# Kernel tuning notes

Hardware: AMD Instinct MI355X
Metric: run time of the kernel (lower is better)

Reference implementation:

```python
import jax, jax.numpy as jnp
import numpy as np
from functools import partial

D_MODEL, N_HEADS, D_FF, KSIZE = 512, 8, 2048, 31
B, S = 8, 1024
EPS = 1e-5

def layer_norm(x, g, b):
    m = jnp.mean(x, axis=-1, keepdims=True)
    v = jnp.mean(jnp.square(x - m), axis=-1, keepdims=True)
    return (x - m) * jax.lax.rsqrt(v + EPS) * g + b

def ffn(x, ln_g, ln_b, w1, b1, w2, b2):
    h = layer_norm(x, ln_g, ln_b)
    h = jax.nn.silu(h @ w1 + b1) @ w2 + b2
    return x + 0.5 * h

def mhsa(x, ln_g, ln_b, wq, bq, wk, bk, wv, bv, wo, bo):
    b_, s_, d_ = x.shape
    dk = d_ // N_HEADS
    h = layer_norm(x, ln_g, ln_b)
    def heads(y):  # (B,S,D) -> (B,H,S,dk)
        return y.reshape(b_, s_, N_HEADS, dk).transpose(0, 2, 1, 3)
    Q, K, V = heads(h @ wq + bq), heads(h @ wk + bk), heads(h @ wv + bv)
    scores = jnp.einsum('bhqd,bhkd->bhqk', Q, K) / jnp.sqrt(jnp.float32(dk)).astype(x.dtype)
    attn = jax.nn.softmax(scores, axis=-1)
    ctx = jnp.einsum('bhqk,bhkd->bhqd', attn, V)
    ctx = ctx.transpose(0, 2, 1, 3).reshape(b_, s_, d_)
    return x + (ctx @ wo + bo)

def conv_module(x, ln_g, ln_b, pw1_w, pw1_b, dw_w, dw_b, bn_g, bn_b, bn_mean, bn_var, pw2_w, pw2_b):
    h = layer_norm(x, ln_g, ln_b)           # (B,S,D)
    h = h @ pw1_w + pw1_b                   # (B,S,2D) pointwise conv1 (k=1)
    a, g = jnp.split(h, 2, axis=-1)
    h = a * jax.nn.sigmoid(g)               # GLU over channel dim
    hc = h.transpose(0, 2, 1)               # (B,D,S)
    # depthwise conv: kernel (D,1,K), groups=D, SAME padding (K odd)
    hc = jax.lax.conv_general_dilated(
        hc, dw_w, window_strides=(1,), padding='SAME',
        dimension_numbers=('NCH', 'OIH', 'NCH'),
        feature_group_count=D_MODEL) + dw_b[None, :, None]
    # BatchNorm1d (eval mode, running stats)
    hc = (hc - bn_mean[None, :, None]) * jax.lax.rsqrt(bn_var + EPS)[None, :, None]
    hc = hc * bn_g[None, :, None] + bn_b[None, :, None]
    hc = jax.nn.silu(hc)
    hc = jnp.einsum('bcs,co->bos', hc, pw2_w) + pw2_b[None, :, None]  # pointwise conv2
    return x + hc.transpose(0, 2, 1)


def setup_inputs() -> dict:
    key = jax.random.key(0)
    ks = iter(jax.random.split(key, 48))
    def w(shape, scale=0.02):
        return (jax.random.normal(next(ks), shape, dtype=jnp.float32) * scale)
    d, f = D_MODEL, D_FF
    inp = {
        'x': jax.random.normal(next(ks), (B, S, d), dtype=jnp.float32),
        # FFN1
        'ffn1_ln_g': jnp.ones((d,)), 'ffn1_ln_b': jnp.zeros((d,)),
        'ffn1_w1': w((d, f)), 'ffn1_b1': jnp.zeros((f,)),
        'ffn1_w2': w((f, d)), 'ffn1_b2': jnp.zeros((d,)),
        # MHSA
        'mhsa_ln_g': jnp.ones((d,)), 'mhsa_ln_b': jnp.zeros((d,)),
        'wq': w((d, d)), 'bq': jnp.zeros((d,)),
        'wk': w((d, d)), 'bk': jnp.zeros((d,)),
        'wv': w((d, d)), 'bv': jnp.zeros((d,)),
        'wo': w((d, d)), 'bo': jnp.zeros((d,)),
        # Conv module
        'conv_ln_g': jnp.ones((d,)), 'conv_ln_b': jnp.zeros((d,)),
        'pw1_w': w((d, 2 * d)), 'pw1_b': jnp.zeros((2 * d,)),
        'dw_w': w((d, 1, KSIZE)), 'dw_b': jnp.zeros((d,)),
        'bn_g': jnp.ones((d,)), 'bn_b': jnp.zeros((d,)),
        'bn_mean': jnp.zeros((d,)), 'bn_var': jnp.ones((d,)),
        'pw2_w': w((d, d)), 'pw2_b': jnp.zeros((d,)),
        # FFN2
        'ffn2_ln_g': jnp.ones((d,)), 'ffn2_ln_b': jnp.zeros((d,)),
        'ffn2_w1': w((d, f)), 'ffn2_b1': jnp.zeros((f,)),
        'ffn2_w2': w((f, d)), 'ffn2_b2': jnp.zeros((d,)),
        # Final LN
        'final_ln_g': jnp.ones((d,)), 'final_ln_b': jnp.zeros((d,)),
    }
    return inp


def reference(x,
              ffn1_ln_g, ffn1_ln_b, ffn1_w1, ffn1_b1, ffn1_w2, ffn1_b2,
              mhsa_ln_g, mhsa_ln_b, wq, bq, wk, bk, wv, bv, wo, bo,
              conv_ln_g, conv_ln_b, pw1_w, pw1_b, dw_w, dw_b,
              bn_g, bn_b, bn_mean, bn_var, pw2_w, pw2_b,
              ffn2_ln_g, ffn2_ln_b, ffn2_w1, ffn2_b1, ffn2_w2, ffn2_b2,
              final_ln_g, final_ln_b):
    h = ffn(x, ffn1_ln_g, ffn1_ln_b, ffn1_w1, ffn1_b1, ffn1_w2, ffn1_b2)
    h = mhsa(h, mhsa_ln_g, mhsa_ln_b, wq, bq, wk, bk, wv, bv, wo, bo)
    h = conv_module(h, conv_ln_g, conv_ln_b, pw1_w, pw1_b, dw_w, dw_b,
                    bn_g, bn_b, bn_mean, bn_var, pw2_w, pw2_b)
    h = ffn(h, ffn2_ln_g, ffn2_ln_b, ffn2_w1, ffn2_b1, ffn2_w2, ffn2_b2)
    return layer_norm(h, final_ln_g, final_ln_b)
```

## Files before the change

### kernel.cpp

```cpp
#include <hip/hip_runtime.h>
#include <hip/hip_bf16.h>
#include <cstddef>

typedef __hip_bfloat16 bf16;
typedef __attribute__((ext_vector_type(8))) short bf16x8;
typedef __attribute__((ext_vector_type(4))) float f32x4;
typedef __attribute__((ext_vector_type(2))) unsigned int u32x2;

static __device__ __forceinline__ float b2f(bf16 v) { return __bfloat162float(v); }
static __device__ __forceinline__ bf16 f2b(float v) { return __float2bfloat16(v); }
static __device__ __forceinline__ float bits2f(unsigned short u) {
    union { unsigned int i; float f; } c; c.i = ((unsigned int)u) << 16; return c.f;
}
static __device__ __forceinline__ unsigned int f2bu(float v) {
    union { bf16 b; unsigned short u; } c; c.b = f2b(v); return (unsigned int)c.u;
}
static __device__ __forceinline__ float ldx(const void* p, size_t i, bool isbf) {
    return isbf ? b2f(((const bf16*)p)[i]) : ((const float*)p)[i];
}
#define GLOAD_LDS16(g, l)                                                            \
    __builtin_amdgcn_global_load_lds((const __attribute__((address_space(1))) unsigned int*)(g), \
                                     (__attribute__((address_space(3))) unsigned int*)(l), 16, 0, 0)

#define LN_EPS 1e-5f

__global__ void detect_kernel(const void* ones, int* flag) {
    unsigned int w = *(const unsigned int*)ones;
    *flag = (w == 0x3F803F80u) ? 1 : 0;
}

__global__ void to_f32_kernel(const void* x, float* __restrict__ y, int n8, const int* flag) {
    bool isbf = (*flag != 0);
    int i = blockIdx.x * blockDim.x + threadIdx.x;
    if (i >= n8) return;
    size_t base = (size_t)i * 8;
    if (isbf) {
        bf16x8 xv = *(const bf16x8*)((const bf16*)x + base);
#pragma unroll
        for (int u = 0; u < 8; ++u) y[base + u] = bits2f((unsigned short)xv[u]);
    } else {
        f32x4 a = *(const f32x4*)((const float*)x + base);
        f32x4 b = *(const f32x4*)((const float*)x + base + 4);
        *(f32x4*)(y + base) = a;
        *(f32x4*)(y + base + 4) = b;
    }
}

__global__ __launch_bounds__(256) void transpose_kernel(const void* __restrict__ W,
                                                        bf16* __restrict__ Wt,
                                                        int K, int M, const int* flag) {
    bool isbf = (*flag != 0);
    __shared__ float ts[32][33];
    int kt0 = blockIdx.x * 32, mt0 = blockIdx.y * 32;
    int x = threadIdx.x, y = threadIdx.y;
    for (int yy = y; yy < 32; yy += 8)
        ts[yy][x] = ldx(W, (size_t)(kt0 + yy) * M + mt0 + x, isbf);
    __syncthreads();
    for (int yy = y; yy < 32; yy += 8)
        Wt[(size_t)(mt0 + yy) * K + kt0 + x] = f2b(ts[x][yy]);
}

__global__ void bpack_kernel(const void* bq, const void* bk, const void* bv,
                             void* out, const int* flag) {
    bool isbf = (*flag != 0);
    int i = blockIdx.x * blockDim.x + threadIdx.x;
    if (i >= 1536) return;
    const void* src = (i < 512) ? bq : ((i < 1024) ? bk : bv);
    float v = ldx(src, i & 511, isbf);
    if (isbf) ((bf16*)out)[i] = f2b(v);
    else      ((float*)out)[i] = v;
}

__global__ __launch_bounds__(256) void vtrans_kernel(const bf16* __restrict__ P,
                                                     bf16* __restrict__ Vt) {
    __shared__ bf16 t[32][33];
    int s0 = blockIdx.x * 32, c0 = blockIdx.y * 32, b = blockIdx.z;
    int x = threadIdx.x, y = threadIdx.y;
    const bf16* Pb = P + (size_t)b * 1024 * 1536 + 1024;
    bf16* Vtb = Vt + (size_t)b * 512 * 1024;
    for (int yy = y; yy < 32; yy += 8)
        t[yy][x] = Pb[(size_t)(s0 + yy) * 1536 + c0 + x];
    __syncthreads();
    for (int yy = y; yy < 32; yy += 8)
        Vtb[(size_t)(c0 + yy) * 1024 + s0 + x] = t[x][yy];
}

__global__ void glu_kernel(const bf16* __restrict__ u, bf16* __restrict__ o, int n8) {
    int i = blockIdx.x * blockDim.x + threadIdx.x;
    if (i >= n8) return;
    size_t base = (size_t)i * 8;
    int t = (int)(base >> 9), c = (int)(base & 511);
    bf16x8 av = *(const bf16x8*)(u + (size_t)t * 1024 + c);
    bf16x8 gv = *(const bf16x8*)(u + (size_t)t * 1024 + 512 + c);
    __attribute__((aligned(16))) bf16 ov[8];
#pragma unroll
    for (int k = 0; k < 8; ++k) {
        float a = bits2f((unsigned short)av[k]);
        float g = bits2f((unsigned short)gv[k]);
        ov[k] = f2b(a / (1.f + __expf(-g)));
    }
    *(bf16x8*)(o + base) = *(bf16x8*)ov;
}

__global__ __launch_bounds__(256) void ln_kernel(const float* __restrict__ X,
                                                 const void* __restrict__ g,
                                                 const void* __restrict__ b,
                                                 bf16* __restrict__ O, const int* flag) {
    bool isbf = (*flag != 0);
    int tid = threadIdx.x, lane = tid & 63, wid = tid >> 6;
    int t = blockIdx.x * 4 + wid;
    const float* x = X + (size_t)t * 512 + lane * 8;
    __attribute__((aligned(16))) float v[8];
    *(f32x4*)&v[0] = *(const f32x4*)x;
    *(f32x4*)&v[4] = *(const f32x4*)(x + 4);
    float s = 0.f, q = 0.f;
#pragma unroll
    for (int u = 0; u < 8; ++u) { s += v[u]; q += v[u] * v[u]; }
#pragma unroll
    for (int m = 1; m < 64; m <<= 1) { s += __shfl_xor(s, m, 64); q += __shfl_xor(q, m, 64); }
    float mean = s * (1.f / 512.f);
    float var  = q * (1.f / 512.f) - mean * mean;
    float sc = rsqrtf(var + LN_EPS);
    __attribute__((aligned(16))) bf16 ov[8];
#pragma unroll
    for (int u = 0; u < 8; ++u)
        ov[u] = f2b((v[u] - mean) * sc * ldx(g, lane * 8 + u, isbf) + ldx(b, lane * 8 + u, isbf));
    *(bf16x8*)(O + (size_t)t * 512 + lane * 8) = *(bf16x8*)ov;
}

__global__ __launch_bounds__(256) void ln_out_kernel(const float* __restrict__ X,
                                                     const void* __restrict__ g,
                                                     const void* __restrict__ b,
                                                     void* __restrict__ O, const int* flag) {
    bool isbf = (*flag != 0);
    int tid = threadIdx.x, lane = tid & 63, wid = tid >> 6;
    int t = blockIdx.x * 4 + wid;
    const float* x = X + (size_t)t * 512 + lane * 8;
    __attribute__((aligned(16))) float v[8];
    *(f32x4*)&v[0] = *(const f32x4*)x;
    *(f32x4*)&v[4] = *(const f32x4*)(x + 4);
    float s = 0.f, q = 0.f;
#pragma unroll
    for (int u = 0; u < 8; ++u) { s += v[u]; q += v[u] * v[u]; }
#pragma unroll
    for (int m = 1; m < 64; m <<= 1) { s += __shfl_xor(s, m, 64); q += __shfl_xor(q, m, 64); }
    float mean = s * (1.f / 512.f);
    float var  = q * (1.f / 512.f) - mean * mean;
    float sc = rsqrtf(var + LN_EPS);
    float r[8];
#pragma unroll
    for (int u = 0; u < 8; ++u)
        r[u] = (v[u] - mean) * sc * ldx(g, lane * 8 + u, isbf) + ldx(b, lane * 8 + u, isbf);
    size_t off = (size_t)t * 512 + lane * 8;
    if (isbf) {
        __attribute__((aligned(16))) bf16 ov[8];
#pragma unroll
        for (int u = 0; u < 8; ++u) ov[u] = f2b(r[u]);
        *(bf16x8*)((bf16*)O + off) = *(bf16x8*)ov;
    } else {
        *(f32x4*)((float*)O + off) = *(f32x4*)&r[0];
        *(f32x4*)((float*)O + off + 4) = *(f32x4*)&r[4];
    }
}

template <int ACT, int RESADD>
__global__ __launch_bounds__(256) void mgemm_kernel(const bf16* __restrict__ A,
                                                    const bf16* __restrict__ Wt,
                                                    const void* __restrict__ bias,
                                                    bf16* __restrict__ Cb,
                                                    float* __restrict__ res, float alpha,
                                                    int lda, int K, int M, const int* flag) {
    bool isbf = (*flag != 0);
    __shared__ short As[128 * 32];
    __shared__ short Bs[128 * 32];
    int tid = threadIdx.x;
    int rowBase = blockIdx.y * 128, colBase = blockIdx.x * 128;
    int ll = tid & 63, wv = tid >> 6;
    int wr = (wv & 1) * 64, wc = (wv >> 1) * 64;
    int lRow = ll & 15, quad = ll >> 4;

    int sR16 = ll >> 2;
    int kseg = (ll & 3) ^ ((ll >> 3) & 3);
    int segF = quad ^ ((lRow >> 1) & 3);

    f32x4 acc[4][4] = {};

    for (int k0 = 0; k0 < K; k0 += 32) {
#pragma unroll
        for (int j = 0; j < 2; ++j) {
            int rT = wv * 32 + j * 16;
            const bf16* ga = A + (size_t)(rowBase + rT + sR16) * lda + k0 + kseg * 8;
            GLOAD_LDS16(ga, &As[rT * 32]);
            const bf16* gb = Wt + (size_t)(colBase + rT + sR16) * K + k0 + kseg * 8;
            GLOAD_LDS16(gb, &Bs[rT * 32]);
        }
        __syncthreads();
        bf16x8 af[4], bfv[4];
#pragma unroll
        for (int i = 0; i < 4; ++i)
            af[i]  = *(const bf16x8*)&As[(wr + i * 16 + lRow) * 32 + segF * 8];
#pragma unroll
        for (int j = 0; j < 4; ++j)
            bfv[j] = *(const bf16x8*)&Bs[(wc + j * 16 + lRow) * 32 + segF * 8];
#pragma unroll
        for (int i = 0; i < 4; ++i)
#pragma unroll
            for (int j = 0; j < 4; ++j)
                acc[i][j] = __builtin_amdgcn_mfma_f32_16x16x32_bf16(af[i], bfv[j], acc[i][j], 0, 0, 0);
        __syncthreads();
    }

#pragma unroll
    for (int j = 0; j < 4; ++j) {
        int col = colBase + wc + j * 16 + lRow;
        float bv = ldx(bias, col, isbf);
#pragma unroll
        for (int i = 0; i < 4; ++i) {
            int r0 = rowBase + wr + i * 16 + quad * 4;
#pragma unroll
            for (int r = 0; r < 4; ++r) {
                float v = acc[i][j][r] + bv;
                if (ACT == 1) v = v / (1.f + __expf(-v));
                int row = r0 + r;
                if (RESADD) res[(size_t)row * 512 + col] += alpha * v;
                else        Cb[(size_t)row * M + col] = f2b(v);
            }
        }
    }
}

__global__ __launch_bounds__(256) void fattn_kernel(bf16* __restrict__ QO,
                                                    const bf16* __restrict__ Vt) {
    __shared__ short Ks[2][64 * 64];
    __shared__ short Vs[2][64 * 64];
    int tid = threadIdx.x, wid = tid >> 6, ll = tid & 63;
    int n = ll & 15, quad = ll >> 4;
    int id = blockIdx.x;
    int ng = gridDim.x >> 4;
    int g = id % ng, j = id / ng;
    int h = g & 7, b = g >> 3;
    size_t rowB = (size_t)b * 1024;
    int q0 = j * 64 + wid * 16;

    const bf16* Qb = QO + rowB * 1536 + h * 64;
    bf16x8 qf0 = *(const bf16x8*)(Qb + (size_t)(q0 + n) * 1536 + quad * 8);
    bf16x8 qf1 = *(const bf16x8*)(Qb + (size_t)(q0 + n) * 1536 + 32 + quad * 8);

    const bf16* Kb = QO + rowB * 1536 + 512 + h * 64;
    const bf16* Vb = Vt + (size_t)b * 512 * 1024 + (size_t)(h * 64) * 1024;

    int rr = ll >> 3;
    int ch = (ll & 7) ^ rr;

    float l = 0.f;
    f32x4 oacc[4] = {};
    int idxA = (((quad & 1) * 32) + n) * 4;
    int idxB = idxA + 64;
    bool hiC = (quad >= 2);
    int nx = n & 7;
    int sl0 = (quad ^ nx) * 8;
    int sl1 = sl0 ^ (4 * 8);

    auto STAGE = [&](int buf, int k0) {
#pragma unroll
        for (int i2 = 0; i2 < 2; ++i2) {
            int r0 = wid * 16 + i2 * 8;
            const bf16* gk = Kb + (size_t)(k0 + r0 + rr) * 1536 + ch * 8;
            GLOAD_LDS16(gk, &Ks[buf][r0 * 64]);
            const bf16* gv = Vb + (size_t)(r0 + rr) * 1024 + k0 + ch * 8;
            GLOAD_LDS16(gv, &Vs[buf][r0 * 64]);
        }
    };

    auto COMPUTE = [&](const short* Kc, const short* Vc) {
#pragma unroll
        for (int s = 0; s < 2; ++s) {
            const short* kb0 = Kc + (s * 32 + n) * 64;
            const short* kb1 = kb0 + 16 * 64;
            f32x4 s0 = {}, s1 = {};
            s0 = __builtin_amdgcn_mfma_f32_16x16x32_bf16(*(const bf16x8*)(kb0 + sl0), qf0, s0, 0, 0, 0);
            s0 = __builtin_amdgcn_mfma_f32_16x16x32_bf16(*(const bf16x8*)(kb0 + sl1), qf1, s0, 0, 0, 0);
            s1 = __builtin_amdgcn_mfma_f32_16x16x32_bf16(*(const bf16x8*)(kb1 + sl0), qf0, s1, 0, 0, 0);
            s1 = __builtin_amdgcn_mfma_f32_16x16x32_bf16(*(const bf16x8*)(kb1 + sl1), qf1, s1, 0, 0, 0);

            float p0[4], p1[4];
#pragma unroll
            for (int r = 0; r < 4; ++r) {
                p0[r] = __expf(s0[r] * 0.125f);
                p1[r] = __expf(s1[r] * 0.125f);
                l += p0[r] + p1[r];
            }

            int p0d0 = (int)(f2bu(p0[0]) | (f2bu(p0[1]) << 16));
            int p0d1 = (int)(f2bu(p0[2]) | (f2bu(p0[3]) << 16));
            int p1d0 = (int)(f2bu(p1[0]) | (f2bu(p1[1]) << 16));
            int p1d1 = (int)(f2bu(p1[2]) | (f2bu(p1[3]) << 16));
            int a0 = __builtin_amdgcn_ds_bpermute(idxA, p0d0);
            int a1 = __builtin_amdgcn_ds_bpermute(idxA, p0d1);
            int a2 = __builtin_amdgcn_ds_bpermute(idxB, p0d0);
            int a3 = __builtin_amdgcn_ds_bpermute(idxB, p0d1);
            int c0 = __builtin_amdgcn_ds_bpermute(idxA, p1d0);
            int c1 = __builtin_amdgcn_ds_bpermute(idxA, p1d1);
            int c2 = __builtin_amdgcn_ds_bpermute(idxB, p1d0);
            int c3 = __builtin_amdgcn_ds_bpermute(idxB, p1d1);
            union { int d[4]; bf16x8 v; } bf;
            bf.d[0] = hiC ? c0 : a0;
            bf.d[1] = hiC ? c1 : a1;
            bf.d[2] = hiC ? c2 : a2;
            bf.d[3] = hiC ? c3 : a3;

            int vsl = ((s * 4 + quad) ^ nx) * 8;
#pragma unroll
            for (int g2 = 0; g2 < 4; ++g2) {
                const short* vp = Vc + (g2 * 16 + n) * 64 + vsl;
                oacc[g2] = __builtin_amdgcn_mfma_f32_16x16x32_bf16(*(const bf16x8*)vp, bf.v, oacc[g2], 0, 0, 0);
            }
        }
    };

    STAGE(0, 0);
    __syncthreads();
    for (int it = 0; it < 16; it += 2) {
        if (it + 1 < 16) STAGE(1, (it + 1) * 64);
        COMPUTE(&Ks[0][0], &Vs[0][0]);
        __syncthreads();
        if (it + 2 < 16) STAGE(0, (it + 2) * 64);
        COMPUTE(&Ks[1][0], &Vs[1][0]);
        __syncthreads();
    }

    l += __shfl_xor(l, 16, 64);
    l += __shfl_xor(l, 32, 64);
    float linv = 1.f / l;
    bf16* op = QO + (rowB + q0 + n) * 1536 + h * 64 + quad * 4;
#pragma unroll
    for (int g2 = 0; g2 < 4; ++g2) {
        union { bf16 b4[4]; u32x2 w; } ou;
#pragma unroll
        for (int r = 0; r < 4; ++r) ou.b4[r] = f2b(oacc[g2][r] * linv);
        *(u32x2*)(op + g2 * 16) = ou.w;
    }
}

__global__ void dwprep_kernel(const void* __restrict__ w, const void* __restrict__ dwb,
                              const void* __restrict__ bng, const void* __restrict__ bnb,
                              const void* __restrict__ bnm, const void* __restrict__ bnv,
                              bf16* __restrict__ wT, float* __restrict__ scl,
                              float* __restrict__ sft, const int* flag) {
    bool isbf = (*flag != 0);
    int c = blockIdx.x * blockDim.x + threadIdx.x;
    if (c >= 512) return;
    for (int k = 0; k < 31; ++k) wT[k * 512 + c] = f2b(ldx(w, (size_t)c * 31 + k, isbf));
    float s = ldx(bng, c, isbf) * rsqrtf(ldx(bnv, c, isbf) + LN_EPS);
    scl[c] = s;
    sft[c] = (ldx(dwb, c, isbf) - ldx(bnm, c, isbf)) * s + ldx(bnb, c, isbf);
}

__global__ __launch_bounds__(256) void dwconv_kernel(const bf16* __restrict__ X,
                                                     const bf16* __restrict__ wT,
                                                     const float* __restrict__ scl,
                                                     const float* __restrict__ sft,
                                                     bf16* __restrict__ Out) {
    __shared__ bf16 wl[31 * 512];
    __shared__ float sl[512], fl[512];
    int tid = threadIdx.x;
    for (int i = tid; i < (31 * 512) / 8; i += 256)
        *(bf16x8*)&wl[i * 8] = *(const bf16x8*)&wT[i * 8];
    sl[tid] = scl[tid]; sl[tid + 256] = scl[tid + 256];
    fl[tid] = sft[tid]; fl[tid + 256] = sft[tid + 256];
    __syncthreads();

    int lane = tid & 63, sg = tid >> 6;
    int c = lane * 8;
    size_t bOff = (size_t)blockIdx.y * 1024 * 512;
    int sb = blockIdx.x * 16 + sg * 4;

    float acc[4][8] = {};
    for (int kk = 0; kk < 34; ++kk) {
        int sp = sb + kk - 15;
        if (sp < 0 || sp >= 1024) continue;
        bf16x8 xr = *(const bf16x8*)(X + bOff + (size_t)sp * 512 + c);
        float xv[8];
#pragma unroll
        for (int u = 0; u < 8; ++u) xv[u] = bits2f((unsigned short)xr[u]);
#pragma unroll
        for (int o = 0; o < 4; ++o) {
            int kw = kk - o;
            if (kw < 0 || kw > 30) continue;
            bf16x8 wv8 = *(const bf16x8*)&wl[kw * 512 + c];
#pragma unroll
            for (int u = 0; u < 8; ++u) acc[o][u] += xv[u] * bits2f((unsigned short)wv8[u]);
        }
    }
#pragma unroll
    for (int o = 0; o < 4; ++o) {
        __attribute__((aligned(16))) bf16 ov[8];
#pragma unroll
        for (int u = 0; u < 8; ++u) {
            float v = acc[o][u] * sl[c + u] + fl[c + u];
            v = v / (1.f + __expf(-v));
            ov[u] = f2b(v);
        }
        *(bf16x8*)(Out + bOff + (size_t)(sb + o) * 512 + c) = *(bf16x8*)ov;
    }
}

extern "C" void kernel_launch(void* const* d_in, const int* in_sizes, int n_in,
                              void* d_out, int out_size, void* d_ws, size_t ws_size,
                              hipStream_t stream) {
    const int B = 8, S = 1024, D = 512, F = 2048, H = 8;
    const int N = B * S;
    const size_t ND = (size_t)N * D;
    if (n_in < 37) return;

    int idx = 0;
    const void* x          = d_in[idx++];
    const void* ffn1_ln_g  = d_in[idx++];
    const void* ffn1_ln_b  = d_in[idx++];
    const void* ffn1_w1    = d_in[idx++];
    const void* ffn1_b1    = d_in[idx++];
    const void* ffn1_w2    = d_in[idx++];
    const void* ffn1_b2    = d_in[idx++];
    const void* mhsa_ln_g  = d_in[idx++];
    const void* mhsa_ln_b  = d_in[idx++];
    const void* wq         = d_in[idx++];
    const void* bq         = d_in[idx++];
    const void* wk         = d_in[idx++];
    const void* bk         = d_in[idx++];
    const void* wv         = d_in[idx++];
    const void* bv         = d_in[idx++];
    const void* wo         = d_in[idx++];
    const void* bo         = d_in[idx++];
    const void* conv_ln_g  = d_in[idx++];
    const void* conv_ln_b  = d_in[idx++];
    const void* pw1_w      = d_in[idx++];
    const void* pw1_b      = d_in[idx++];
    const void* dw_w       = d_in[idx++];
    const void* dw_b       = d_in[idx++];
    const void* bn_g       = d_in[idx++];
    const void* bn_b       = d_in[idx++];
    const void* bn_mean    = d_in[idx++];
    const void* bn_var     = d_in[idx++];
    const void* pw2_w      = d_in[idx++];
    const void* pw2_b      = d_in[idx++];
    const void* ffn2_ln_g  = d_in[idx++];
    const void* ffn2_ln_b  = d_in[idx++];
    const void* ffn2_w1    = d_in[idx++];
    const void* ffn2_b1    = d_in[idx++];
    const void* ffn2_w2    = d_in[idx++];
    const void* ffn2_b2    = d_in[idx++];
    const void* final_ln_g = d_in[idx++];
    const void* final_ln_b = d_in[idx++];

    const size_t MB = 1024 * 1024;
    char* wsb  = (char*)d_ws;
    int*  flag = (int*)wsb;
    float* res = (float*)(wsb + 1024);
    bf16*  wt  = (bf16*)(wsb + 1024 + ND * 4);
    char*  dwr = wsb + 1024 + ND * 4 + 4 * MB;
    bf16*  dwT  = (bf16*)dwr;
    float* dscl = (float*)(dwr + 32768);
    float* dsft = dscl + 512;
    void*  qkvB = (void*)(dwr + 40960);
    char*  scr = dwr + 65536;
    size_t base = 1024 + ND * 4 + 4 * MB + 65536;
    size_t scrB = (ws_size > base) ? ws_size - base : 0;
    int ffnRows = (scrB >= 32 * MB) ? 8192 : ((scrB >= 8 * MB) ? 2048 : 1024);
    int bI      = (scrB >= 32 * MB) ? 8    : ((scrB >= 8 * MB) ? 2    : 1);
    int cI      = (scrB >= 32 * MB) ? 8    : ((scrB >= 8 * MB) ? 2    : 1);

    bf16* h = (bf16*)d_out;

    detect_kernel<<<1, 1, 0, stream>>>(ffn1_ln_g, flag);
    to_f32_kernel<<<(int)(ND / 8 / 256), 256, 0, stream>>>(x, res, (int)(ND / 8), flag);

    auto run_ffn = [&](const void* lg, const void* lb, const void* w1, const void* b1,
                       const void* w2, const void* b2) {
        bf16* w1t = wt;
        bf16* w2t = wt + (size_t)D * F;
        transpose_kernel<<<dim3(D / 32, F / 32), dim3(32, 8), 0, stream>>>(w1, w1t, D, F, flag);
        transpose_kernel<<<dim3(F / 32, D / 32), dim3(32, 8), 0, stream>>>(w2, w2t, F, D, flag);
        ln_kernel<<<N / 4, 256, 0, stream>>>(res, lg, lb, h, flag);
        bf16* mid = (bf16*)scr;
        for (int r0 = 0; r0 < N; r0 += ffnRows) {
            mgemm_kernel<1, 0><<<dim3(F / 128, ffnRows / 128), 256, 0, stream>>>(
                h + (size_t)r0 * D, w1t, b1, mid, nullptr, 0.f, D, D, F, flag);
            mgemm_kernel<0, 1><<<dim3(D / 128, ffnRows / 128), 256, 0, stream>>>(
                mid, w2t, b2, nullptr, res + (size_t)r0 * D, 0.5f, F, F, D, flag);
        }
    };

    run_ffn(ffn1_ln_g, ffn1_ln_b, ffn1_w1, ffn1_b1, ffn1_w2, ffn1_b2);

    {
        bf16* qt = wt;
        bf16* kt = wt + (size_t)D * D;
        bf16* vt = wt + 2 * (size_t)D * D;
        bf16* ot = wt + 3 * (size_t)D * D;
        transpose_kernel<<<dim3(D / 32, D / 32), dim3(32, 8), 0, stream>>>(wq, qt, D, D, flag);
        transpose_kernel<<<dim3(D / 32, D / 32), dim3(32, 8), 0, stream>>>(wk, kt, D, D, flag);
        transpose_kernel<<<dim3(D / 32, D / 32), dim3(32, 8), 0, stream>>>(wv, vt, D, D, flag);
        transpose_kernel<<<dim3(D / 32, D / 32), dim3(32, 8), 0, stream>>>(wo, ot, D, D, flag);
        bpack_kernel<<<6, 256, 0, stream>>>(bq, bk, bv, qkvB, flag);
        ln_kernel<<<N / 4, 256, 0, stream>>>(res, mhsa_ln_g, mhsa_ln_b, h, flag);
        for (int b = 0; b < B; b += bI) {
            int rows = bI * S;
            bf16* packed = (bf16*)scr;
            bf16* Vt = packed + (size_t)rows * 1536;
            const bf16* Ah = h + (size_t)b * S * D;
            mgemm_kernel<0, 0><<<dim3(1536 / 128, rows / 128), 256, 0, stream>>>(
                Ah, qt, qkvB, packed, nullptr, 0.f, D, D, 1536, flag);
            vtrans_kernel<<<dim3(S / 32, D / 32, bI), dim3(32, 8), 0, stream>>>(packed, Vt);
            fattn_kernel<<<dim3(bI * H * 16), 256, 0, stream>>>(packed, Vt);
            mgemm_kernel<0, 1><<<dim3(D / 128, rows / 128), 256, 0, stream>>>(
                packed, ot, bo, nullptr, res + (size_t)b * S * D, 1.0f, 1536, D, D, flag);
        }
    }

    {
        bf16* p1t = wt;
        bf16* p2t = wt + (size_t)D * 2 * D;
        transpose_kernel<<<dim3(D / 32, (2 * D) / 32), dim3(32, 8), 0, stream>>>(pw1_w, p1t, D, 2 * D, flag);
        transpose_kernel<<<dim3(D / 32, D / 32), dim3(32, 8), 0, stream>>>(pw2_w, p2t, D, D, flag);
        dwprep_kernel<<<2, 256, 0, stream>>>(dw_w, dw_b, bn_g, bn_b, bn_mean, bn_var, dwT, dscl, dsft, flag);
        ln_kernel<<<N / 4, 256, 0, stream>>>(res, conv_ln_g, conv_ln_b, h, flag);
        for (int b = 0; b < B; b += cI) {
            int rows = cI * S;
            bf16* u  = (bf16*)scr;
            bf16* hg = u + (size_t)rows * 2 * D;
            bf16* dw = hg + (size_t)rows * D;
            const bf16* Ah = h + (size_t)b * S * D;
            mgemm_kernel<0, 0><<<dim3((2 * D) / 128, rows / 128), 256, 0, stream>>>(
                Ah, p1t, pw1_b, u, nullptr, 0.f, D, D, 2 * D, flag);
            glu_kernel<<<(rows * D / 8) / 256, 256, 0, stream>>>(u, hg, rows * D / 8);
            dwconv_kernel<<<dim3(S / 16, cI), 256, 0, stream>>>(hg, dwT, dscl, dsft, dw);
            mgemm_kernel<0, 1><<<dim3(D / 128, rows / 128), 256, 0, stream>>>(
                dw, p2t, pw2_b, nullptr, res + (size_t)b * S * D, 1.0f, D, D, D, flag);
        }
    }

    run_ffn(ffn2_ln_g, ffn2_ln_b, ffn2_w1, ffn2_b1, ffn2_w2, ffn2_b2);

    ln_out_kernel<<<N / 4, 256, 0, stream>>>(res, final_ln_g, final_ln_b, d_out, flag);
}
```

Baseline: 601.1 us.

## Double-buffer GEMM LDS tiles and split-K residual GEMMs with atomic accumulation

The bf16 MFMA GEMM now uses two LDS buffers so the next K-slice is loaded while the current one is multiplied. It also adds a split-K mode for the residual-add GEMMs: blockIdx.z takes a K range, only the first split adds the bias, and partial results are added into the fp32 residual with atomicAdd. This targets the low block counts of the N=512 output GEMMs and exposed load latency. In exchange it doubles LDS per block, adds atomic traffic, and makes the fp32 summation order nondeterministic.

```diff
diff --git a/kernel.cpp b/kernel.cpp
--- a/kernel.cpp
+++ b/kernel.cpp
@@ -163,7 +163,7 @@
     }
 }
 
-template <int ACT, int RESADD>
+template <int ACT, int RESADD, int KS>
 __global__ __launch_bounds__(256) void mgemm_kernel(const bf16* __restrict__ A,
                                                     const bf16* __restrict__ Wt,
                                                     const void* __restrict__ bias,
@@ -171,8 +171,8 @@
                                                     float* __restrict__ res, float alpha,
                                                     int lda, int K, int M, const int* flag) {
     bool isbf = (*flag != 0);
-    __shared__ short As[128 * 32];
-    __shared__ short Bs[128 * 32];
+    __shared__ short As[2][128 * 32];
+    __shared__ short Bs[2][128 * 32];
     int tid = threadIdx.x;
     int rowBase = blockIdx.y * 128, colBase = blockIdx.x * 128;
     int ll = tid & 63, wv = tid >> 6;
@@ -183,25 +183,35 @@
     int kseg = (ll & 3) ^ ((ll >> 3) & 3);
     int segF = quad ^ ((lRow >> 1) & 3);
 
+    int kPer = K / gridDim.z;
+    int kBeg = blockIdx.z * kPer;
+    int nSteps = kPer >> 5;
+
     f32x4 acc[4][4] = {};
 
-    for (int k0 = 0; k0 < K; k0 += 32) {
+    auto STAGE = [&](int buf, int k0) {
 #pragma unroll
         for (int j = 0; j < 2; ++j) {
             int rT = wv * 32 + j * 16;
             const bf16* ga = A + (size_t)(rowBase + rT + sR16) * lda + k0 + kseg * 8;
-            GLOAD_LDS16(ga, &As[rT * 32]);
+            GLOAD_LDS16(ga, &As[buf][rT * 32]);
             const bf16* gb = Wt + (size_t)(colBase + rT + sR16) * K + k0 + kseg * 8;
-            GLOAD_LDS16(gb, &Bs[rT * 32]);
-        }
-        __syncthreads();
+            GLOAD_LDS16(gb, &Bs[buf][rT * 32]);
+        }
+    };
+
+    STAGE(0, kBeg);
+    __syncthreads();
+    for (int it = 0; it < nSteps; ++it) {
+        int cur = it & 1;
+        if (it + 1 < nSteps) STAGE(cur ^ 1, kBeg + (it + 1) * 32);
         bf16x8 af[4], bfv[4];
 #pragma unroll
         for (int i = 0; i < 4; ++i)
-            af[i]  = *(const bf16x8*)&As[(wr + i * 16 + lRow) * 32 + segF * 8];
+            af[i]  = *(const bf16x8*)&As[cur][(wr + i * 16 + lRow) * 32 + segF * 8];
 #pragma unroll
         for (int j = 0; j < 4; ++j)
-            bfv[j] = *(const bf16x8*)&Bs[(wc + j * 16 + lRow) * 32 + segF * 8];
+            bfv[j] = *(const bf16x8*)&Bs[cur][(wc + j * 16 + lRow) * 32 + segF * 8];
 #pragma unroll
         for (int i = 0; i < 4; ++i)
 #pragma unroll
@@ -213,7 +223,7 @@
 #pragma unroll
     for (int j = 0; j < 4; ++j) {
         int col = colBase + wc + j * 16 + lRow;
-        float bv = ldx(bias, col, isbf);
+        float bv = (KS != 0 && blockIdx.z != 0) ? 0.f : ldx(bias, col, isbf);
 #pragma unroll
         for (int i = 0; i < 4; ++i) {
             int r0 = rowBase + wr + i * 16 + quad * 4;
@@ -222,8 +232,12 @@
                 float v = acc[i][j][r] + bv;
                 if (ACT == 1) v = v / (1.f + __expf(-v));
                 int row = r0 + r;
-                if (RESADD) res[(size_t)row * 512 + col] += alpha * v;
-                else        Cb[(size_t)row * M + col] = f2b(v);
+                if (RESADD) {
+                    if (KS) atomicAdd(&res[(size_t)row * 512 + col], alpha * v);
+                    else    res[(size_t)row * 512 + col] += alpha * v;
+                } else {
+                    Cb[(size_t)row * M + col] = f2b(v);
+                }
             }
         }
     }
@@ -483,9 +497,9 @@
         ln_kernel<<<N / 4, 256, 0, stream>>>(res, lg, lb, h, flag);
         bf16* mid = (bf16*)scr;
         for (int r0 = 0; r0 < N; r0 += ffnRows) {
-            mgemm_kernel<1, 0><<<dim3(F / 128, ffnRows / 128), 256, 0, stream>>>(
+            mgemm_kernel<1, 0, 0><<<dim3(F / 128, ffnRows / 128, 1), 256, 0, stream>>>(
                 h + (size_t)r0 * D, w1t, b1, mid, nullptr, 0.f, D, D, F, flag);
-            mgemm_kernel<0, 1><<<dim3(D / 128, ffnRows / 128), 256, 0, stream>>>(
+            mgemm_kernel<0, 1, 1><<<dim3(D / 128, ffnRows / 128, 4), 256, 0, stream>>>(
                 mid, w2t, b2, nullptr, res + (size_t)r0 * D, 0.5f, F, F, D, flag);
         }
     };
@@ -508,11 +522,11 @@
             bf16* packed = (bf16*)scr;
             bf16* Vt = packed + (size_t)rows * 1536;
             const bf16* Ah = h + (size_t)b * S * D;
-            mgemm_kernel<0, 0><<<dim3(1536 / 128, rows / 128), 256, 0, stream>>>(
+            mgemm_kernel<0, 0, 0><<<dim3(1536 / 128, rows / 128, 1), 256, 0, stream>>>(
                 Ah, qt, qkvB, packed, nullptr, 0.f, D, D, 1536, flag);
             vtrans_kernel<<<dim3(S / 32, D / 32, bI), dim3(32, 8), 0, stream>>>(packed, Vt);
             fattn_kernel<<<dim3(bI * H * 16), 256, 0, stream>>>(packed, Vt);
-            mgemm_kernel<0, 1><<<dim3(D / 128, rows / 128), 256, 0, stream>>>(
+            mgemm_kernel<0, 1, 1><<<dim3(D / 128, rows / 128, 2), 256, 0, stream>>>(
                 packed, ot, bo, nullptr, res + (size_t)b * S * D, 1.0f, 1536, D, D, flag);
         }
     }
@@ -530,11 +544,11 @@
             bf16* hg = u + (size_t)rows * 2 * D;
             bf16* dw = hg + (size_t)rows * D;
             const bf16* Ah = h + (size_t)b * S * D;
-            mgemm_kernel<0, 0><<<dim3((2 * D) / 128, rows / 128), 256, 0, stream>>>(
+            mgemm_kernel<0, 0, 0><<<dim3((2 * D) / 128, rows / 128, 1), 256, 0, stream>>>(
                 Ah, p1t, pw1_b, u, nullptr, 0.f, D, D, 2 * D, flag);
             glu_kernel<<<(rows * D / 8) / 256, 256, 0, stream>>>(u, hg, rows * D / 8);
             dwconv_kernel<<<dim3(S / 16, cI), 256, 0, stream>>>(hg, dwT, dscl, dsft, dw);
-            mgemm_kernel<0, 1><<<dim3(D / 128, rows / 128), 256, 0, stream>>>(
+            mgemm_kernel<0, 1, 1><<<dim3(D / 128, rows / 128, 2), 256, 0, stream>>>(
                 dw, p2t, pw2_b, nullptr, res + (size_t)b * S * D, 1.0f, D, D, D, flag);
         }
     }
```

Measured after the change: 679.1 us. +13.0%, slower.
